# Kernel optimization log

Hardware: AMD Instinct MI355X
Metric: run time of the kernel (lower is better)

Reference implementation:

```python
import jax, jax.numpy as jnp
import numpy as np

S, B, V, E, H, T = 256, 32, 50000, 300, 256, 32  # seq, batch, vocab, emb, lstm hidden, num_tags


def _lstm_dir(x, w_ih, w_hh, b_ih, b_hh, reverse):
    # x: [S, B, in]; gates in PyTorch order i, f, g, o
    Bm, Hm = x.shape[1], w_hh.shape[1]
    def step(carry, xt):
        h, c = carry
        g = xt @ w_ih.T + b_ih + h @ w_hh.T + b_hh  # [B, 4H]
        i, f, gg, o = jnp.split(g, 4, axis=-1)
        c = jax.nn.sigmoid(f) * c + jax.nn.sigmoid(i) * jnp.tanh(gg)
        h = jax.nn.sigmoid(o) * jnp.tanh(c)
        return (h, c), h
    init = (jnp.zeros((Bm, Hm), x.dtype), jnp.zeros((Bm, Hm), x.dtype))
    _, hs = jax.lax.scan(step, init, x, reverse=reverse)
    return hs  # [S, B, H]


def _crf_loss(em, tags, start, trans, end):
    # em: [S, B, T]; torchcrf log-likelihood, reduction='sum', full mask
    bidx = jnp.arange(em.shape[1])
    # numerator (gold path score)
    emit = jnp.take_along_axis(em, tags[:, :, None], axis=2)[..., 0].sum(0)  # [B]
    tr = trans[tags[:-1], tags[1:]].sum(0)  # [B]
    num = start[tags[0]] + emit + tr + end[tags[-1]]
    # denominator (forward algorithm)
    def step(alpha, e):
        alpha = jax.nn.logsumexp(alpha[:, :, None] + trans[None] + e[:, None, :], axis=1)
        return alpha, None
    alpha0 = start[None] + em[0]  # [B, T]
    alpha, _ = jax.lax.scan(step, alpha0, em[1:])
    logZ = jax.nn.logsumexp(alpha + end[None], axis=-1)  # [B]
    return -(num - logZ).sum()


def _viterbi(em, start, trans, end):
    def step(s, e):
        cand = s[:, :, None] + trans[None]           # [B, T_prev, T_cur]
        return cand.max(1) + e, cand.argmax(1)        # score [B,T], backptr [B,T]
    score0 = start[None] + em[0]
    score, hist = jax.lax.scan(step, score0, em[1:])  # hist: [S-1, B, T]
    last = jnp.argmax(score + end[None], axis=-1)     # [B]
    def back(tag, bp):
        prev = jnp.take_along_axis(bp, tag[:, None], axis=1)[:, 0]
        return prev, prev
    _, path_head = jax.lax.scan(back, last, hist, reverse=True)  # [S-1, B]
    return jnp.concatenate([path_head, last[None]], axis=0).astype(jnp.int32)  # [S, B]


def setup_inputs():
    key = jax.random.key(0)
    ks = jax.random.split(key, 32)
    def n(k, shape, s=0.1):
        return (jax.random.normal(k, shape, jnp.float32) * s)
    inp = {
        'words': jax.random.randint(ks[0], (S, B), 0, V),
        'chars': jax.random.randint(ks[1], (S, B, 16), 0, 100),
        'tags': jax.random.randint(ks[2], (S, B), 0, T),
        'emb_table': n(ks[3], (V, E)),
        'fc_w': n(ks[4], (T, 2 * H), float(np.sqrt(2.0 / (T + 2 * H)))),
        'fc_b': n(ks[5], (T,), float(np.sqrt(1.0 / T))),
        'crf_start': n(ks[6], (T,)),
        'crf_end': n(ks[7], (T,)),
        'crf_trans': n(ks[8], (T, T)),
    }
    i = 9
    for l, din in ((0, E), (1, 2 * H)):
        for d in ('f', 'b'):
            inp[f'w_ih_l{l}{d}'] = n(ks[i], (4 * H, din)); i += 1
            inp[f'w_hh_l{l}{d}'] = n(ks[i], (4 * H, H)); i += 1
            inp[f'b_ih_l{l}{d}'] = n(ks[i], (4 * H,)); i += 1
            inp[f'b_hh_l{l}{d}'] = n(ks[i], (4 * H,)); i += 1
    return inp


def reference(words, chars, tags, emb_table, fc_w, fc_b, crf_start, crf_end, crf_trans,
              w_ih_l0f, w_hh_l0f, b_ih_l0f, b_hh_l0f,
              w_ih_l0b, w_hh_l0b, b_ih_l0b, b_hh_l0b,
              w_ih_l1f, w_hh_l1f, b_ih_l1f, b_hh_l1f,
              w_ih_l1b, w_hh_l1b, b_ih_l1b, b_hh_l1b):
    # chars / char CNN are unused in the original forward()
    x = emb_table[words]                                   # [S, B, E]
    h0 = jnp.concatenate([
        _lstm_dir(x, w_ih_l0f, w_hh_l0f, b_ih_l0f, b_hh_l0f, False),
        _lstm_dir(x, w_ih_l0b, w_hh_l0b, b_ih_l0b, b_hh_l0b, True)], axis=-1)
    h1 = jnp.concatenate([
        _lstm_dir(h0, w_ih_l1f, w_hh_l1f, b_ih_l1f, b_hh_l1f, False),
        _lstm_dir(h0, w_ih_l1b, w_hh_l1b, b_ih_l1b, b_hh_l1b, True)], axis=-1)  # [S, B, 2H]
    em = h1 @ fc_w.T + fc_b                                # emissions [S, B, T]
    crf_out = _viterbi(em, crf_start, crf_trans, crf_end)  # [S, B] int32
    crf_loss = _crf_loss(em, tags, crf_start, crf_trans, crf_end)
    return crf_out, crf_loss
```

## Files before the change

### kernel.cpp

```cpp
#include <hip/hip_runtime.h>
#include <stdint.h>

#define S_ 256
#define B_ 32
#define H_ 256
#define G4_ 1024
#define HXW (16*132)

typedef short bf16x8 __attribute__((ext_vector_type(8)));
typedef float f32x4  __attribute__((ext_vector_type(4)));

__device__ __forceinline__ unsigned f2bf(float f){
  unsigned u = __float_as_uint(f);
  return (u + 0x7fffu + ((u >> 16) & 1u)) >> 16;
}
__device__ __forceinline__ float bfl(unsigned u){ return __uint_as_float(u << 16); }
__device__ __forceinline__ float bfh(unsigned u){ return __uint_as_float(u & 0xffff0000u); }
__device__ __forceinline__ float sigf(float x){ return 1.0f / (1.0f + __expf(-x)); }
__device__ __forceinline__ float thf(float x){
  x = fminf(fmaxf(x, -15.0f), 15.0f);
  float e = __expf(2.0f * x);
  return (e - 1.0f) / (e + 1.0f);
}

__device__ __forceinline__ int hval_ok(unsigned long long v){
  return (((unsigned)v & (unsigned)(v >> 32)) & 0x40004000u) == 0x40004000u;
}

__global__ __launch_bounds__(320) void k_prep(const int* __restrict__ words,
                                              const float* __restrict__ emb,
                                              unsigned short* __restrict__ x,
                                              unsigned* __restrict__ hbuf0){
  int row = blockIdx.x;
  int e = threadIdx.x;
  int w = words[row];
  x[row * 320 + e] = (e < 300) ? (unsigned short)f2bf(emb[w * 300 + e]) : 0;
  if (e < 256) hbuf0[row * 256 + e] = 0;
}

__global__ __launch_bounds__(256) void k_packw(
    const float* __restrict__ w0f, const float* __restrict__ w0b,
    const float* __restrict__ w1f, const float* __restrict__ w1b,
    const float* __restrict__ fw,
    unsigned short* __restrict__ wb0f, unsigned short* __restrict__ wb0b,
    unsigned short* __restrict__ wb1f, unsigned short* __restrict__ wb1b,
    unsigned short* __restrict__ fcwb){
  int r = blockIdx.x, tid = threadIdx.x;
  if (r < 2048){
    int rr = r & 1023;
    const float* src = (r < 1024) ? w0f : w0b;
    unsigned short* dst = (r < 1024) ? wb0f : wb0b;
    for (int e = tid; e < 320; e += 256)
      dst[rr * 320 + e] = (e < 300) ? (unsigned short)f2bf(src[rr * 300 + e]) : 0;
  } else if (r < 4096){
    int rr = r & 1023;
    const float* src = (r < 3072) ? w1f : w1b;
    unsigned short* dst = (r < 3072) ? wb1f : wb1b;
    for (int e = tid; e < 512; e += 256)
      dst[rr * 512 + e] = (unsigned short)f2bf(src[rr * 512 + e]);
  } else {
    int rr = r - 4096;
    for (int e = tid; e < 512; e += 256)
      fcwb[rr * 512 + e] = (unsigned short)f2bf(fw[rr * 512 + e]);
  }
}

__global__ __launch_bounds__(256) void k_gemm_bf2(
    const unsigned short* __restrict__ A, int lda, int nSteps,
    const unsigned short* __restrict__ Bf, const unsigned short* __restrict__ Bb,
    const float* __restrict__ b1f, const float* __restrict__ b2f,
    const float* __restrict__ b1b, const float* __restrict__ b2b,
    float* __restrict__ Cf, float* __restrict__ Cb){
  const int z = blockIdx.z;
  const unsigned short* __restrict__ B = z ? Bb : Bf;
  const float* __restrict__ bias1 = z ? b1b : b1f;
  const float* __restrict__ bias2 = z ? b2b : b2f;
  float* __restrict__ C = z ? Cb : Cf;

  __shared__ __align__(16) unsigned As[64 * 20];
  __shared__ __align__(16) unsigned Bs[128 * 20];
  const int tid = threadIdx.x;
  const int w = tid >> 6, lane = tid & 63;
  const int quad = lane >> 4, coln = lane & 15;
  const int m0 = blockIdx.y * 64, n0 = blockIdx.x * 128;

  f32x4 acc[8];
  #pragma unroll
  for (int i = 0; i < 8; ++i){ acc[i][0]=0.f; acc[i][1]=0.f; acc[i][2]=0.f; acc[i][3]=0.f; }

  for (int kt = 0; kt < nSteps; ++kt){
    int k0 = kt * 32;
    __syncthreads();
    {
      int row = tid >> 2, part = tid & 3;
      *(uint4*)&As[row * 20 + part * 4] =
          *(const uint4*)(A + (size_t)(m0 + row) * lda + k0 + part * 8);
    }
    #pragma unroll
    for (int i = 0; i < 2; ++i){
      int idx = tid + 256 * i;
      int row = idx >> 2, part = idx & 3;
      *(uint4*)&Bs[row * 20 + part * 4] =
          *(const uint4*)(B + (size_t)(n0 + row) * lda + k0 + part * 8);
    }
    __syncthreads();
    union { uint4 q; bf16x8 v; } au;
    au.q = *(const uint4*)&As[(w * 16 + coln) * 20 + quad * 4];
    #pragma unroll
    for (int nt = 0; nt < 8; ++nt){
      union { uint4 q; bf16x8 v; } bu;
      bu.q = *(const uint4*)&Bs[(nt * 16 + coln) * 20 + quad * 4];
      acc[nt] = __builtin_amdgcn_mfma_f32_16x16x32_bf16(au.v, bu.v, acc[nt], 0, 0, 0);
    }
  }
  #pragma unroll
  for (int nt = 0; nt < 8; ++nt){
    int col = n0 + nt * 16 + coln;
    float bs = bias1[col] + bias2[col];
    #pragma unroll
    for (int reg = 0; reg < 4; ++reg)
      C[(size_t)(m0 + w * 16 + quad * 4 + reg) * 1024 + col] = acc[nt][reg] + bs;
  }
}

__global__ __launch_bounds__(256, 1) void k_lstm2(
    const float* __restrict__ Gf, const float* __restrict__ Gb,
    const float* __restrict__ Whf, const float* __restrict__ Whb,
    unsigned* __restrict__ hbuf,
    unsigned short* __restrict__ Hout)
{
  __shared__ __align__(16) unsigned hx[2 * HXW];
  const int wg  = blockIdx.x;
  const int dir = wg >> 3, n = (wg >> 1) & 3, bh = wg & 1;
  const float* __restrict__ G  = dir ? Gb : Gf;
  const float* __restrict__ Wh = dir ? Whb : Whf;
  const int tid  = threadIdx.x;
  const int w    = tid >> 6;
  const int lane = tid & 63;
  const int quad = lane >> 4, coln = lane & 15;

  bf16x8 Wr[32];
  #pragma unroll
  for (int ks = 0; ks < 8; ++ks){
    #pragma unroll
    for (int gt = 0; gt < 4; ++gt){
      const float* wp = Wh + (size_t)(gt * 256 + (n << 6) + (w << 4) + coln) * 256
                        + ks * 32 + quad * 8;
      float4 a = *(const float4*)wp;
      float4 b = *(const float4*)(wp + 4);
      union { unsigned u[4]; bf16x8 v; } tu;
      tu.u[0] = f2bf(a.x) | (f2bf(a.y) << 16);
      tu.u[1] = f2bf(a.z) | (f2bf(a.w) << 16);
      tu.u[2] = f2bf(b.x) | (f2bf(b.y) << 16);
      tu.u[3] = f2bf(b.z) | (f2bf(b.w) << 16);
      Wr[ks * 4 + gt] = tu.v;
    }
  }

  const int gu  = (n << 6) + (w << 4) + coln;
  const int mrw = quad << 2;

  float c0 = 0.f, c1 = 0.f, c2 = 0.f, c3 = 0.f;

  for (int t = 0; t < 256; ++t){
    int s = dir ? (255 - t) : t;
    f32x4 acc[4];
    #pragma unroll
    for (int gt = 0; gt < 4; ++gt){
      const float* gp = G + (size_t)(s * 32 + bh * 16 + mrw) * 1024 + gt * 256 + gu;
      f32x4 a;
      a[0] = gp[0]; a[1] = gp[1024]; a[2] = gp[2048]; a[3] = gp[3072];
      acc[gt] = a;
    }
    unsigned* hxr = &hx[(t & 1) * HXW];
    if (t > 0){
      const unsigned* hb = hbuf + (((size_t)(t - 1) * 2 + dir) * 2 + bh) * 2048;
      int row = tid >> 4, kk = tid & 15;
      int n1 = (n + 1) & 3, n2 = (n + 2) & 3, n3 = (n + 3) & 3;
      const unsigned long long* p1 =
          (const unsigned long long*)(hb + row * 128 + n1 * 32 + kk * 2);
      const unsigned long long* p2 =
          (const unsigned long long*)(hb + row * 128 + n2 * 32 + kk * 2);
      const unsigned long long* p3 =
          (const unsigned long long*)(hb + row * 128 + n3 * 32 + kk * 2);
      unsigned long long v1, v2, v3;
      do {
        v1 = __hip_atomic_load(p1, __ATOMIC_RELAXED, __HIP_MEMORY_SCOPE_AGENT);
        v2 = __hip_atomic_load(p2, __ATOMIC_RELAXED, __HIP_MEMORY_SCOPE_AGENT);
        v3 = __hip_atomic_load(p3, __ATOMIC_RELAXED, __HIP_MEMORY_SCOPE_AGENT);
      } while (!(hval_ok(v1) && hval_ok(v2) && hval_ok(v3)));
      hxr[row * 132 + n1 * 32 + kk * 2]     = (unsigned)v1 & 0xBFFFBFFFu;
      hxr[row * 132 + n1 * 32 + kk * 2 + 1] = (unsigned)(v1 >> 32) & 0xBFFFBFFFu;
      hxr[row * 132 + n2 * 32 + kk * 2]     = (unsigned)v2 & 0xBFFFBFFFu;
      hxr[row * 132 + n2 * 32 + kk * 2 + 1] = (unsigned)(v2 >> 32) & 0xBFFFBFFFu;
      hxr[row * 132 + n3 * 32 + kk * 2]     = (unsigned)v3 & 0xBFFFBFFFu;
      hxr[row * 132 + n3 * 32 + kk * 2 + 1] = (unsigned)(v3 >> 32) & 0xBFFFBFFFu;
      __syncthreads();
      #pragma unroll
      for (int ks = 0; ks < 8; ++ks){
        union { uint4 q; bf16x8 v; } tu;
        tu.q = *(const uint4*)&hxr[coln * 132 + ks * 16 + quad * 4];
        #pragma unroll
        for (int gt = 0; gt < 4; ++gt)
          acc[gt] = __builtin_amdgcn_mfma_f32_16x16x32_bf16(tu.v, Wr[ks * 4 + gt],
                                                            acc[gt], 0, 0, 0);
      }
    }
    unsigned* hxw = &hx[((t + 1) & 1) * HXW];
    unsigned* hw  = hbuf + (((size_t)t * 2 + dir) * 2 + bh) * 2048;
    float cc[4] = {c0, c1, c2, c3};
    #pragma unroll
    for (int reg = 0; reg < 4; ++reg){
      float gi = sigf(acc[0][reg]);
      float gf = sigf(acc[1][reg]);
      float gg = thf (acc[2][reg]);
      float go = sigf(acc[3][reg]);
      float cv = gf * cc[reg] + gi * gg;
      cc[reg] = cv;
      float hv = go * thf(cv);
      unsigned hb16 = f2bf(hv);
      unsigned other = (unsigned)__shfl_xor((int)hb16, 1);
      if (!(coln & 1)){
        unsigned pair = hb16 | (other << 16);
        hxw[(mrw + reg) * 132 + (gu >> 1)] = pair;
        if (t < 255)
          __hip_atomic_store(hw + (mrw + reg) * 128 + (gu >> 1),
                             pair | 0x40004000u,
                             __ATOMIC_RELAXED, __HIP_MEMORY_SCOPE_AGENT);
      }
      Hout[(size_t)(s * 32 + bh * 16 + mrw + reg) * 512 + dir * 256 + gu] =
          (unsigned short)hb16;
    }
    c0 = cc[0]; c1 = cc[1]; c2 = cc[2]; c3 = cc[3];
  }
}

__global__ __launch_bounds__(64) void k_fc(const unsigned short* __restrict__ h1,
                                           const unsigned short* __restrict__ fw,
                                           const float* __restrict__ fb,
                                           float* __restrict__ em){
  int row = blockIdx.x;
  int lane = threadIdx.x;
  int tag = lane & 31, half = lane >> 5;
  const uint4* hp = (const uint4*)(h1 + (size_t)row * 512 + half * 256);
  const uint4* wp = (const uint4*)(fw + (size_t)tag * 512 + half * 256);
  float acc = 0.0f;
  #pragma unroll 8
  for (int i = 0; i < 32; ++i){
    uint4 h = hp[i], v = wp[i];
    acc += bfl(h.x) * bfl(v.x) + bfh(h.x) * bfh(v.x)
         + bfl(h.y) * bfl(v.y) + bfh(h.y) * bfh(v.y)
         + bfl(h.z) * bfl(v.z) + bfh(h.z) * bfh(v.z)
         + bfl(h.w) * bfl(v.w) + bfh(h.w) * bfh(v.w);
  }
  acc += __shfl_down(acc, 32);
  if (half == 0) em[row * 32 + tag] = acc + fb[tag];
}

__global__ __launch_bounds__(64) void k_crf(const float* __restrict__ em,
                                            const int* __restrict__ tags,
                                            const float* __restrict__ start,
                                            const float* __restrict__ trans,
                                            const float* __restrict__ endv,
                                            int* __restrict__ path,
                                            float* __restrict__ lossb){
  __shared__ float tr[1024];
  __shared__ float sc[32], sc2[32];
  __shared__ unsigned char bp[255][32];
  int b = blockIdx.x & 31, mode = blockIdx.x >> 5;
  int t = threadIdx.x;
  for (int i = t; i < 1024; i += 64) tr[i] = trans[i];
  if (t < 32) sc[t] = start[t] + em[b * 32 + t];
  __syncthreads();
  if (mode == 0){
    for (int s = 1; s < 256; ++s){
      if (t < 32){
        float best = -1e30f; int bi = 0;
        for (int p = 0; p < 32; ++p){
          float v = sc[p] + tr[p * 32 + t];
          if (v > best){ best = v; bi = p; }
        }
        sc2[t] = best + em[(s * 32 + b) * 32 + t];
        bp[s - 1][t] = (unsigned char)bi;
      }
      __syncthreads();
      if (t < 32) sc[t] = sc2[t];
      __syncthreads();
    }
    if (t == 0){
      float best = -1e30f; int bi = 0;
      for (int p = 0; p < 32; ++p){
        float v = sc[p] + endv[p];
        if (v > best){ best = v; bi = p; }
      }
      int cur = bi;
      path[255 * 32 + b] = cur;
      for (int s = 254; s >= 0; --s){
        cur = bp[s][cur];
        path[s * 32 + b] = cur;
      }
    }
  } else {
    for (int s = 1; s < 256; ++s){
      if (t < 32){
        float m = -1e30f;
        for (int p = 0; p < 32; ++p){ float v = sc[p] + tr[p * 32 + t]; m = fmaxf(m, v); }
        float ss = 0.0f;
        for (int p = 0; p < 32; ++p){ ss += __expf(sc[p] + tr[p * 32 + t] - m); }
        sc2[t] = m + __logf(ss) + em[(s * 32 + b) * 32 + t];
      }
      __syncthreads();
      if (t < 32) sc[t] = sc2[t];
      __syncthreads();
    }
    float nsum = 0.0f;
    for (int s = t; s < 256; s += 64){
      int tg = tags[s * 32 + b];
      nsum += em[(s * 32 + b) * 32 + tg];
      if (s == 0) nsum += start[tg];
      else        nsum += tr[tags[(s - 1) * 32 + b] * 32 + tg];
      if (s == 255) nsum += endv[tg];
    }
    #pragma unroll
    for (int off = 32; off >= 1; off >>= 1) nsum += __shfl_down(nsum, off);
    if (t == 0){
      float m = -1e30f;
      for (int p = 0; p < 32; ++p) m = fmaxf(m, sc[p] + endv[p]);
      float ss = 0.0f;
      for (int p = 0; p < 32; ++p) ss += __expf(sc[p] + endv[p] - m);
      lossb[b] = m + __logf(ss) - nsum;
    }
  }
}

__global__ __launch_bounds__(64) void k_final(const float* __restrict__ lossb,
                                              float* __restrict__ outp){
  float v = (threadIdx.x < 32) ? lossb[threadIdx.x] : 0.0f;
  #pragma unroll
  for (int off = 32; off >= 1; off >>= 1) v += __shfl_down(v, off);
  if (threadIdx.x == 0) outp[0] = v;
}

extern "C" void kernel_launch(void* const* d_in, const int* in_sizes, int n_in,
                              void* d_out, int out_size, void* d_ws, size_t ws_size,
                              hipStream_t stream){
  const int*   words  = (const int*)d_in[0];
  const int*   tags   = (const int*)d_in[2];
  const float* emb    = (const float*)d_in[3];
  const float* fcw    = (const float*)d_in[4];
  const float* fcb    = (const float*)d_in[5];
  const float* cstart = (const float*)d_in[6];
  const float* cend   = (const float*)d_in[7];
  const float* ctrans = (const float*)d_in[8];
  const float* w_ih[4] = {(const float*)d_in[9],  (const float*)d_in[13],
                          (const float*)d_in[17], (const float*)d_in[21]};
  const float* w_hh[4] = {(const float*)d_in[10], (const float*)d_in[14],
                          (const float*)d_in[18], (const float*)d_in[22]};
  const float* b_ih[4] = {(const float*)d_in[11], (const float*)d_in[15],
                          (const float*)d_in[19], (const float*)d_in[23]};
  const float* b_hh[4] = {(const float*)d_in[12], (const float*)d_in[16],
                          (const float*)d_in[20], (const float*)d_in[24]};

  char* base = (char*)d_ws;
  unsigned short* x    = (unsigned short*)base;
  float* Gf            = (float*)(base + 5242880);
  float* Gb            = (float*)(base + 38797312);
  unsigned short* h0   = (unsigned short*)(base + 72351744);
  unsigned short* h1   = (unsigned short*)(base + 80740352);
  unsigned short* wb0f = (unsigned short*)(base + 89128960);
  unsigned short* wb0b = (unsigned short*)(base + 89784320);
  unsigned short* wb1f = (unsigned short*)(base + 90439680);
  unsigned short* wb1b = (unsigned short*)(base + 91488256);
  unsigned short* fcwb = (unsigned short*)(base + 92536832);
  float* lossb         = (float*)(base + 92569600);
  float* em            = Gf;
  unsigned* hbuf0 = (unsigned*)h1;
  unsigned* hbuf1 = (unsigned*)h0;

  k_prep<<<8192, 320, 0, stream>>>(words, emb, x, hbuf0);
  k_packw<<<4128, 256, 0, stream>>>(w_ih[0], w_ih[1], w_ih[2], w_ih[3], fcw,
                                    wb0f, wb0b, wb1f, wb1b, fcwb);

  k_gemm_bf2<<<dim3(8, 128, 2), 256, 0, stream>>>(x, 320, 10, wb0f, wb0b,
                                                  b_ih[0], b_hh[0], b_ih[1], b_hh[1],
                                                  Gf, Gb);
  k_lstm2<<<16, 256, 0, stream>>>(Gf, Gb, w_hh[0], w_hh[1], hbuf0, h0);

  k_gemm_bf2<<<dim3(8, 128, 2), 256, 0, stream>>>(h0, 512, 16, wb1f, wb1b,
                                                  b_ih[2], b_hh[2], b_ih[3], b_hh[3],
                                                  Gf, Gb);
  k_lstm2<<<16, 256, 0, stream>>>(Gf, Gb, w_hh[2], w_hh[3], hbuf1, h1);

  k_fc<<<8192, 64, 0, stream>>>(h1, fcwb, fcb, em);

  k_crf<<<64, 64, 0, stream>>>(em, tags, cstart, ctrans, cend, (int*)d_out, lossb);
  k_final<<<1, 64, 0, stream>>>(lossb, ((float*)d_out) + (out_size - 1));
}
```

Before: 1.498 ms.

## Merge prep and weight-pack kernels, use MFMA for FC, split CRF reductions

Fuses the embedding gather and weight-packing kernels into one launch to save a launch. Rewrites the FC emission projection as an MFMA bf16 GEMM, with the weights staged in shared memory and 64 rows per block. The CRF Viterbi and forward loops now split the 32 predecessor states across both halves of the wavefront and combine the halves with shuffles, which halves the serial per-step work. The LSTM kernels, where most of the time goes, are unchanged, so the overall gain is likely small.

```diff
diff --git a/kernel.cpp b/kernel.cpp
--- a/kernel.cpp
+++ b/kernel.cpp
@@ -27,40 +27,40 @@
   return (((unsigned)v & (unsigned)(v >> 32)) & 0x40004000u) == 0x40004000u;
 }
 
-__global__ __launch_bounds__(320) void k_prep(const int* __restrict__ words,
-                                              const float* __restrict__ emb,
-                                              unsigned short* __restrict__ x,
-                                              unsigned* __restrict__ hbuf0){
-  int row = blockIdx.x;
-  int e = threadIdx.x;
-  int w = words[row];
-  x[row * 320 + e] = (e < 300) ? (unsigned short)f2bf(emb[w * 300 + e]) : 0;
-  if (e < 256) hbuf0[row * 256 + e] = 0;
-}
-
-__global__ __launch_bounds__(256) void k_packw(
+__global__ __launch_bounds__(320) void k_prep(
+    const int* __restrict__ words, const float* __restrict__ emb,
+    unsigned short* __restrict__ x, unsigned* __restrict__ hbuf0,
     const float* __restrict__ w0f, const float* __restrict__ w0b,
     const float* __restrict__ w1f, const float* __restrict__ w1b,
     const float* __restrict__ fw,
     unsigned short* __restrict__ wb0f, unsigned short* __restrict__ wb0b,
     unsigned short* __restrict__ wb1f, unsigned short* __restrict__ wb1b,
     unsigned short* __restrict__ fcwb){
-  int r = blockIdx.x, tid = threadIdx.x;
+  int blk = blockIdx.x, tid = threadIdx.x;
+  if (blk < 8192){
+    int row = blk;
+    int e = tid;
+    int w = words[row];
+    x[row * 320 + e] = (e < 300) ? (unsigned short)f2bf(emb[w * 300 + e]) : 0;
+    if (e < 256) hbuf0[row * 256 + e] = 0;
+    return;
+  }
+  int r = blk - 8192;
   if (r < 2048){
     int rr = r & 1023;
     const float* src = (r < 1024) ? w0f : w0b;
     unsigned short* dst = (r < 1024) ? wb0f : wb0b;
-    for (int e = tid; e < 320; e += 256)
+    for (int e = tid; e < 320; e += 320)
       dst[rr * 320 + e] = (e < 300) ? (unsigned short)f2bf(src[rr * 300 + e]) : 0;
   } else if (r < 4096){
     int rr = r & 1023;
     const float* src = (r < 3072) ? w1f : w1b;
     unsigned short* dst = (r < 3072) ? wb1f : wb1b;
-    for (int e = tid; e < 512; e += 256)
+    for (int e = tid; e < 512; e += 320)
       dst[rr * 512 + e] = (unsigned short)f2bf(src[rr * 512 + e]);
   } else {
     int rr = r - 4096;
-    for (int e = tid; e < 512; e += 256)
+    for (int e = tid; e < 512; e += 320)
       fcwb[rr * 512 + e] = (unsigned short)f2bf(fw[rr * 512 + e]);
   }
 }
@@ -235,26 +235,45 @@
   }
 }
 
-__global__ __launch_bounds__(64) void k_fc(const unsigned short* __restrict__ h1,
-                                           const unsigned short* __restrict__ fw,
-                                           const float* __restrict__ fb,
-                                           float* __restrict__ em){
-  int row = blockIdx.x;
-  int lane = threadIdx.x;
-  int tag = lane & 31, half = lane >> 5;
-  const uint4* hp = (const uint4*)(h1 + (size_t)row * 512 + half * 256);
-  const uint4* wp = (const uint4*)(fw + (size_t)tag * 512 + half * 256);
-  float acc = 0.0f;
-  #pragma unroll 8
-  for (int i = 0; i < 32; ++i){
-    uint4 h = hp[i], v = wp[i];
-    acc += bfl(h.x) * bfl(v.x) + bfh(h.x) * bfh(v.x)
-         + bfl(h.y) * bfl(v.y) + bfh(h.y) * bfh(v.y)
-         + bfl(h.z) * bfl(v.z) + bfh(h.z) * bfh(v.z)
-         + bfl(h.w) * bfl(v.w) + bfh(h.w) * bfh(v.w);
-  }
-  acc += __shfl_down(acc, 32);
-  if (half == 0) em[row * 32 + tag] = acc + fb[tag];
+__global__ __launch_bounds__(256) void k_fc(const unsigned short* __restrict__ h1,
+                                            const unsigned short* __restrict__ fw,
+                                            const float* __restrict__ fb,
+                                            float* __restrict__ em){
+  __shared__ __align__(16) unsigned Bs[32 * 260];
+  const int tid = threadIdx.x;
+  const int w = tid >> 6, lane = tid & 63;
+  const int quad = lane >> 4, coln = lane & 15;
+  const int m0 = blockIdx.x * 64;
+
+  for (int i = tid; i < 2048; i += 256){
+    int r = i >> 6, part = i & 63;
+    *(uint4*)&Bs[r * 260 + part * 4] = *(const uint4*)(fw + r * 512 + part * 8);
+  }
+  __syncthreads();
+
+  f32x4 acc[2];
+  acc[0][0]=0.f; acc[0][1]=0.f; acc[0][2]=0.f; acc[0][3]=0.f;
+  acc[1][0]=0.f; acc[1][1]=0.f; acc[1][2]=0.f; acc[1][3]=0.f;
+  const unsigned short* arow = h1 + (size_t)(m0 + w * 16 + coln) * 512;
+  #pragma unroll
+  for (int ks = 0; ks < 16; ++ks){
+    union { uint4 q; bf16x8 v; } au;
+    au.q = *(const uint4*)(arow + ks * 32 + quad * 8);
+    #pragma unroll
+    for (int nt = 0; nt < 2; ++nt){
+      union { uint4 q; bf16x8 v; } bu;
+      bu.q = *(const uint4*)&Bs[(nt * 16 + coln) * 260 + ks * 16 + quad * 4];
+      acc[nt] = __builtin_amdgcn_mfma_f32_16x16x32_bf16(au.v, bu.v, acc[nt], 0, 0, 0);
+    }
+  }
+  #pragma unroll
+  for (int nt = 0; nt < 2; ++nt){
+    int col = nt * 16 + coln;
+    float bias = fb[col];
+    #pragma unroll
+    for (int reg = 0; reg < 4; ++reg)
+      em[(size_t)(m0 + w * 16 + quad * 4 + reg) * 32 + col] = acc[nt][reg] + bias;
+  }
 }
 
 __global__ __launch_bounds__(64) void k_crf(const float* __restrict__ em,
@@ -269,19 +288,25 @@
   __shared__ unsigned char bp[255][32];
   int b = blockIdx.x & 31, mode = blockIdx.x >> 5;
   int t = threadIdx.x;
+  int tt = t & 31, half = t >> 5;
   for (int i = t; i < 1024; i += 64) tr[i] = trans[i];
   if (t < 32) sc[t] = start[t] + em[b * 32 + t];
   __syncthreads();
   if (mode == 0){
     for (int s = 1; s < 256; ++s){
-      if (t < 32){
-        float best = -1e30f; int bi = 0;
-        for (int p = 0; p < 32; ++p){
-          float v = sc[p] + tr[p * 32 + t];
-          if (v > best){ best = v; bi = p; }
-        }
-        sc2[t] = best + em[(s * 32 + b) * 32 + t];
-        bp[s - 1][t] = (unsigned char)bi;
+      float best = -1e30f; int bi = 0;
+      #pragma unroll
+      for (int q = 0; q < 16; ++q){
+        int p = half * 16 + q;
+        float v = sc[p] + tr[p * 32 + tt];
+        if (v > best){ best = v; bi = p; }
+      }
+      float ob = __shfl_xor(best, 32);
+      int   oi = __shfl_xor(bi, 32);
+      if (half == 0){
+        if (ob > best){ best = ob; bi = oi; }
+        sc2[tt] = best + em[(s * 32 + b) * 32 + tt];
+        bp[s - 1][tt] = (unsigned char)bi;
       }
       __syncthreads();
       if (t < 32) sc[t] = sc2[t];
@@ -302,12 +327,24 @@
     }
   } else {
     for (int s = 1; s < 256; ++s){
-      if (t < 32){
-        float m = -1e30f;
-        for (int p = 0; p < 32; ++p){ float v = sc[p] + tr[p * 32 + t]; m = fmaxf(m, v); }
-        float ss = 0.0f;
-        for (int p = 0; p < 32; ++p){ ss += __expf(sc[p] + tr[p * 32 + t] - m); }
-        sc2[t] = m + __logf(ss) + em[(s * 32 + b) * 32 + t];
+      float m = -1e30f;
+      #pragma unroll
+      for (int q = 0; q < 16; ++q){
+        int p = half * 16 + q;
+        m = fmaxf(m, sc[p] + tr[p * 32 + tt]);
+      }
+      float ss = 0.0f;
+      #pragma unroll
+      for (int q = 0; q < 16; ++q){
+        int p = half * 16 + q;
+        ss += __expf(sc[p] + tr[p * 32 + tt] - m);
+      }
+      float om = __shfl_xor(m, 32);
+      float os = __shfl_xor(ss, 32);
+      if (half == 0){
+        float M = fmaxf(m, om);
+        float SS = ss * __expf(m - M) + os * __expf(om - M);
+        sc2[tt] = M + __logf(SS) + em[(s * 32 + b) * 32 + tt];
       }
       __syncthreads();
       if (t < 32) sc[t] = sc2[t];
@@ -377,8 +414,8 @@
   unsigned* hbuf0 = (unsigned*)h1;
   unsigned* hbuf1 = (unsigned*)h0;
 
-  k_prep<<<8192, 320, 0, stream>>>(words, emb, x, hbuf0);
-  k_packw<<<4128, 256, 0, stream>>>(w_ih[0], w_ih[1], w_ih[2], w_ih[3], fcw,
+  k_prep<<<12320, 320, 0, stream>>>(words, emb, x, hbuf0,
+                                    w_ih[0], w_ih[1], w_ih[2], w_ih[3], fcw,
                                     wb0f, wb0b, wb1f, wb1b, fcwb);
 
   k_gemm_bf2<<<dim3(8, 128, 2), 256, 0, stream>>>(x, 320, 10, wb0f, wb0b,
@@ -391,7 +428,7 @@
                                                   Gf, Gb);
   k_lstm2<<<16, 256, 0, stream>>>(Gf, Gb, w_hh[2], w_hh[3], hbuf1, h1);
 
-  k_fc<<<8192, 64, 0, stream>>>(h1, fcwb, fcb, em);
+  k_fc<<<128, 256, 0, stream>>>(h1, fcwb, fcb, em);
 
   k_crf<<<64, 64, 0, stream>>>(em, tags, cstart, ctrans, cend, (int*)d_out, lossb);
   k_final<<<1, 64, 0, stream>>>(lossb, ((float*)d_out) + (out_size - 1));
```

New measurement: 1.413 ms. 1.06x faster.
